# Optimization experiments

Measured on AMD Instinct MI355X. Metric: run time of the kernel, lower is better.

The kernel has to match this reference:

```python
import jax, jax.numpy as jnp
import numpy as np

N_NODES = 50000
N_EDGES = 800000
IN_DIM = 64
HID = 64
NUM_GRAPHS = 512


def _gcn_conv(x, W, b, row, col, norm, n):
    # PyG GCNConv: h = x @ W; out[col] += norm * h[row]; out += b
    h = x @ W  # [N, HID]
    msg = h[row] * norm[:, None]  # [E', HID]
    out = jax.ops.segment_sum(msg, col, num_segments=n)
    return out + b


def setup_inputs() -> dict:
    key = jax.random.key(0)
    ks = jax.random.split(key, 12)
    x = jax.random.normal(ks[0], (N_NODES, IN_DIM), dtype=jnp.float32)
    edge_index = jax.random.randint(ks[1], (2, N_EDGES), 0, N_NODES, dtype=jnp.int64)
    batch = jnp.sort(jax.random.randint(ks[2], (N_NODES,), 0, NUM_GRAPHS, dtype=jnp.int64))
    s = 0.05
    W1 = jax.random.normal(ks[3], (IN_DIM, HID), dtype=jnp.float32) * s
    b1 = jnp.zeros((HID,), dtype=jnp.float32)
    W2 = jax.random.normal(ks[4], (HID, HID), dtype=jnp.float32) * s
    b2 = jnp.zeros((HID,), dtype=jnp.float32)
    W3 = jax.random.normal(ks[5], (HID, HID), dtype=jnp.float32) * s
    b3 = jnp.zeros((HID,), dtype=jnp.float32)
    lin_W = jax.random.normal(ks[6], (HID, 1), dtype=jnp.float32) * s
    lin_b = jnp.zeros((1,), dtype=jnp.float32)
    return {"x": x, "W1": W1, "b1": b1, "W2": W2, "b2": b2, "W3": W3,
            "b3": b3, "lin_W": lin_W, "lin_b": lin_b,
            "edge_index": edge_index, "batch": batch}


def reference(x, W1, b1, W2, b2, W3, b3, lin_W, lin_b, edge_index, batch):
    n = x.shape[0]
    # add self-loops (GCNConv default add_self_loops=True)
    loop = jnp.arange(n, dtype=edge_index.dtype)
    row = jnp.concatenate([edge_index[0], loop])  # source
    col = jnp.concatenate([edge_index[1], loop])  # target (aggregation index)
    # symmetric degree normalization: deg over targets with unit weights
    deg = jax.ops.segment_sum(jnp.ones_like(col, dtype=x.dtype), col, num_segments=n)
    dinv = jnp.where(deg > 0, jax.lax.rsqrt(deg), 0.0)
    norm = dinv[row] * dinv[col]  # [E+N]

    h = jax.nn.relu(_gcn_conv(x, W1, b1, row, col, norm, n))
    h = jax.nn.relu(_gcn_conv(h, W2, b2, row, col, norm, n))
    h = _gcn_conv(h, W3, b3, row, col, norm, n)

    # global_mean_pool over batch ids
    sums = jax.ops.segment_sum(h, batch, num_segments=NUM_GRAPHS)
    cnt = jax.ops.segment_sum(jnp.ones((n,), dtype=h.dtype), batch, num_segments=NUM_GRAPHS)
    pooled = sums / jnp.maximum(cnt, 1.0)[:, None]
    # dropout p=0.5 is identity in eval mode
    return pooled @ lin_W + lin_b  # [NUM_GRAPHS, 1]
```

## Files before the change

kernel.cpp:

```cpp
#include <hip/hip_runtime.h>
#include <hip/hip_fp16.h>

#define NN 50000
#define NE 800000
#define HD 64
#define NG 512
#define NBK 196
#define NBL 196
#define M_CNT (NBK * NBL)
#define NBS 151
#define GEMM_BLOCKS 3125


__global__ __launch_bounds__(256) void bucket_count(const int* __restrict__ col,
                                                    const int* __restrict__ batch,
                                                    int* __restrict__ cnt,
                                                    int* __restrict__ counts,
                                                    int* __restrict__ beg,
                                                    int* __restrict__ endx,
                                                    float* __restrict__ pooled) {
    __shared__ int hist[256];
    int tid = threadIdx.x, blk = blockIdx.x;
    hist[tid] = 0;
    __syncthreads();
    int base = blk * 4096;
#pragma unroll
    for (int k = 0; k < 16; ++k) {
        int e = base + k * 256 + tid;
        if (e < NE) {
            int c = col[e];
            atomicAdd(&cnt[c], 1);
            atomicAdd(&hist[c >> 8], 1);
        }
    }
    int t = blk * 256 + tid;
    if (t < NG * HD) pooled[t] = 0.f;
    if (t < NN) {
        int g = batch[t];
        if (t == 0 || batch[t - 1] != g) beg[g] = t;
        if (t == NN - 1 || batch[t + 1] != g) endx[g] = t + 1;
    }
    __syncthreads();
    if (tid < NBK) counts[tid * NBL + blk] = hist[tid];
}

__global__ __launch_bounds__(256) void mscan(const int* __restrict__ src,
                                             int* __restrict__ dst) {
    __shared__ int ws[4];
    __shared__ int wsum[4];
    __shared__ int spref;
    int tid = threadIdx.x, lane = tid & 63, wid = tid >> 6;
    int lim = blockIdx.x * 256;
    int ps = 0;
    for (int k = tid; k < lim; k += 256) ps += src[k];
#pragma unroll
    for (int off = 32; off > 0; off >>= 1) ps += __shfl_down(ps, off, 64);
    if (lane == 0) wsum[wid] = ps;
    int i = lim + tid;
    int v = (i < M_CNT) ? src[i] : 0;
    int inc = v;
#pragma unroll
    for (int off = 1; off < 64; off <<= 1) {
        int t = __shfl_up(inc, off, 64);
        if (lane >= off) inc += t;
    }
    if (lane == 63) ws[wid] = inc;
    __syncthreads();
    if (tid == 0) spref = wsum[0] + wsum[1] + wsum[2] + wsum[3];
    __syncthreads();
    int woff = 0;
    for (int k = 0; k < wid; ++k) woff += ws[k];
    if (i < M_CNT) dst[i] = spref + woff + inc - v;
}

__global__ __launch_bounds__(256) void gemm1_scatter(const float* __restrict__ x,
                                                     const float* __restrict__ W1,
                                                     const int* __restrict__ cnt,
                                                     __half* __restrict__ h16,
                                                     const int* __restrict__ row,
                                                     const int* __restrict__ col,
                                                     const int* __restrict__ counts_ex,
                                                     unsigned* __restrict__ packed,
                                                     int* __restrict__ rowptr,
                                                     float* __restrict__ dinv) {
    if (blockIdx.x < GEMM_BLOCKS) {
        __shared__ float Is[16][64];
        int t = threadIdx.x;
        int c = t & 63, r4 = t >> 6;
        float wcol[64];
#pragma unroll
        for (int k = 0; k < 64; ++k) wcol[k] = W1[k * HD + c];
        int row0 = blockIdx.x * 16;
        float d0 = rsqrtf((float)(cnt[row0 + r4 + 0] + 1));
        float d1 = rsqrtf((float)(cnt[row0 + r4 + 4] + 1));
        float d2 = rsqrtf((float)(cnt[row0 + r4 + 8] + 1));
        float d3 = rsqrtf((float)(cnt[row0 + r4 + 12] + 1));
        for (int i = t; i < 16 * 64; i += 256)
            Is[i >> 6][i & 63] = x[(row0 + (i >> 6)) * HD + (i & 63)];
        __syncthreads();
        float a0 = 0.f, a1 = 0.f, a2 = 0.f, a3 = 0.f;
        const float4* i0p = (const float4*)&Is[r4 + 0][0];
        const float4* i1p = (const float4*)&Is[r4 + 4][0];
        const float4* i2p = (const float4*)&Is[r4 + 8][0];
        const float4* i3p = (const float4*)&Is[r4 + 12][0];
#pragma unroll
        for (int q = 0; q < 16; ++q) {
            float4 i0 = i0p[q], i1 = i1p[q], i2 = i2p[q], i3 = i3p[q];
            float w0 = wcol[4 * q + 0], w1 = wcol[4 * q + 1];
            float w2 = wcol[4 * q + 2], w3 = wcol[4 * q + 3];
            a0 += i0.x * w0; a0 += i0.y * w1; a0 += i0.z * w2; a0 += i0.w * w3;
            a1 += i1.x * w0; a1 += i1.y * w1; a1 += i1.z * w2; a1 += i1.w * w3;
            a2 += i2.x * w0; a2 += i2.y * w1; a2 += i2.z * w2; a2 += i2.w * w3;
            a3 += i3.x * w0; a3 += i3.y * w1; a3 += i3.z * w2; a3 += i3.w * w3;
        }
        h16[(row0 + r4 + 0) * HD + c] = __float2half(d0 * a0);
        h16[(row0 + r4 + 4) * HD + c] = __float2half(d1 * a1);
        h16[(row0 + r4 + 8) * HD + c] = __float2half(d2 * a2);
        h16[(row0 + r4 + 12) * HD + c] = __float2half(d3 * a3);
    } else if (blockIdx.x < GEMM_BLOCKS + NBL) {
        __shared__ int cur[256];
        int tid = threadIdx.x, blk = blockIdx.x - GEMM_BLOCKS;
        cur[tid] = 0;
        __syncthreads();
        int base = blk * 4096;
#pragma unroll
        for (int k = 0; k < 16; ++k) {
            int e = base + k * 256 + tid;
            if (e < NE) {
                int c = col[e], r = row[e];
                int b = c >> 8;
                int lpos = atomicAdd(&cur[b], 1);
                int pos = counts_ex[b * NBL + blk] + lpos;
                packed[pos] = (unsigned)r | ((unsigned)(c & 255) << 16);
            }
        }
    } else {
        __shared__ int ws[4];
        int b = blockIdx.x - (GEMM_BLOCKS + NBL);
        int tid = threadIdx.x, lane = tid & 63, wid = tid >> 6;
        int node = b * 256 + tid;
        int v = (node < NN) ? cnt[node] : 0;
        int inc = v;
#pragma unroll
        for (int off = 1; off < 64; off <<= 1) {
            int t = __shfl_up(inc, off, 64);
            if (lane >= off) inc += t;
        }
        if (lane == 63) ws[wid] = inc;
        __syncthreads();
        int woff = 0;
        for (int k = 0; k < wid; ++k) woff += ws[k];
        int s0 = counts_ex[b * NBL];
        if (node <= NN) rowptr[node] = s0 + woff + inc - v;
        if (node < NN) dinv[node] = rsqrtf((float)(v + 1));
    }
}

__global__ __launch_bounds__(256) void csr_fill(const unsigned* __restrict__ packed,
                                                const int* __restrict__ counts_ex,
                                                const int* __restrict__ rowptr,
                                                int* __restrict__ esrc) {
    __shared__ int lrp[256];
    __shared__ int cur[256];
    int bkt = blockIdx.x, tid = threadIdx.x;
    int s = counts_ex[bkt * NBL];
    int e = (bkt == NBK - 1) ? NE : counts_ex[(bkt + 1) * NBL];
    int node = bkt * 256 + tid;
    lrp[tid] = (node < NN) ? rowptr[node] : 0;
    cur[tid] = 0;
    __syncthreads();
    for (int j = s + tid; j < e; j += 256) {
        unsigned p = packed[j];
        int lc = (p >> 16) & 255;
        int slot = lrp[lc] + atomicAdd(&cur[lc], 1);
        esrc[slot] = (int)(p & 0xFFFF);
    }
}

template <bool POOL>
__global__ __launch_bounds__(256) void gather_fx(const __half* __restrict__ hp,
                                                 const int* __restrict__ rowptr,
                                                 const int* __restrict__ esrc,
                                                 const float* __restrict__ dinv,
                                                 const float* __restrict__ b,
                                                 const float* __restrict__ Wnext,
                                                 __half* __restrict__ hnext,
                                                 const int* __restrict__ batch,
                                                 float* __restrict__ pooled) {
    __shared__ float rowbuf[4][64];
    int tid = threadIdx.x, lane = tid & 63, wid = tid >> 6;
    int p = lane >> 5, c = lane & 31;
    int node = __builtin_amdgcn_readfirstlane(blockIdx.x * 4 + wid);
    const __half2* hv = (const __half2*)hp;

    float di = dinv[node];
    float2 self = __half22float2(hv[node * 32 + c]);
    float2 bb = ((const float2*)b)[c];

    float wcol[POOL ? 1 : 64];
    if (!POOL) {
#pragma unroll
        for (int k = 0; k < 64; ++k) wcol[k] = Wnext[k * HD + lane];
    }

    int s = rowptr[node], e = rowptr[node + 1];
    float2 acc = {0.f, 0.f};
    int j = s;
    for (; j + 8 <= e; j += 8) {
        int t0 = esrc[j + 0], t1 = esrc[j + 1], t2 = esrc[j + 2], t3 = esrc[j + 3];
        int t4 = esrc[j + 4], t5 = esrc[j + 5], t6 = esrc[j + 6], t7 = esrc[j + 7];
        int a0 = p ? t1 : t0;
        int a1 = p ? t3 : t2;
        int a2 = p ? t5 : t4;
        int a3 = p ? t7 : t6;
        float2 f0 = __half22float2(hv[a0 * 32 + c]);
        float2 f1 = __half22float2(hv[a1 * 32 + c]);
        float2 f2 = __half22float2(hv[a2 * 32 + c]);
        float2 f3 = __half22float2(hv[a3 * 32 + c]);
        acc.x += (f0.x + f1.x) + (f2.x + f3.x);
        acc.y += (f0.y + f1.y) + (f2.y + f3.y);
    }
    if (j < e) {
        int t0 = esrc[j + 0] & 0xFFFF, t1 = esrc[j + 1] & 0xFFFF;
        int t2 = esrc[j + 2] & 0xFFFF, t3 = esrc[j + 3] & 0xFFFF;
        int t4 = esrc[j + 4] & 0xFFFF, t5 = esrc[j + 5] & 0xFFFF;
        int t6 = esrc[j + 6] & 0xFFFF, t7 = esrc[j + 7] & 0xFFFF;
        int i0 = j + p, i1 = j + 2 + p, i2 = j + 4 + p, i3 = j + 6 + p;
        int a0 = p ? t1 : t0;
        int a1 = p ? t3 : t2;
        int a2 = p ? t5 : t4;
        int a3 = p ? t7 : t6;
        a0 = (i0 < e) ? a0 : t0;
        a1 = (i1 < e) ? a1 : t0;
        a2 = (i2 < e) ? a2 : t0;
        a3 = (i3 < e) ? a3 : t0;
        float m0 = (i0 < e) ? 1.f : 0.f;
        float m1 = (i1 < e) ? 1.f : 0.f;
        float m2 = (i2 < e) ? 1.f : 0.f;
        float m3 = (i3 < e) ? 1.f : 0.f;
        float2 f0 = __half22float2(hv[a0 * 32 + c]);
        float2 f1 = __half22float2(hv[a1 * 32 + c]);
        float2 f2 = __half22float2(hv[a2 * 32 + c]);
        float2 f3 = __half22float2(hv[a3 * 32 + c]);
        acc.x += m0 * f0.x + m1 * f1.x + m2 * f2.x + m3 * f3.x;
        acc.y += m0 * f0.y + m1 * f1.y + m2 * f2.y + m3 * f3.y;
    }
    acc.x += __shfl_xor(acc.x, 32, 64);
    acc.y += __shfl_xor(acc.y, 32, 64);

    if (POOL) {
        if (p == 0) {
            float vx = di * (acc.x + self.x) + bb.x;
            float vy = di * (acc.y + self.y) + bb.y;
            int g = batch[node];
            atomicAdd(&pooled[g * HD + 2 * c], vx);
            atomicAdd(&pooled[g * HD + 2 * c + 1], vy);
        }
    } else {
        if (p == 0) {
            rowbuf[wid][2 * c]     = fmaxf(di * (acc.x + self.x) + bb.x, 0.f);
            rowbuf[wid][2 * c + 1] = fmaxf(di * (acc.y + self.y) + bb.y, 0.f);
        }
        float outc = 0.f;
        const float4* rb4 = (const float4*)&rowbuf[wid][0];
#pragma unroll
        for (int jj = 0; jj < 16; ++jj) {
            float4 r = rb4[jj];
            outc += r.x * wcol[4 * jj + 0] + r.y * wcol[4 * jj + 1]
                  + r.z * wcol[4 * jj + 2] + r.w * wcol[4 * jj + 3];
        }
        hnext[(size_t)node * HD + lane] = __float2half(di * outc);
    }
}

__global__ __launch_bounds__(64) void final_kernel(const float* __restrict__ pooled,
                                                   const int* __restrict__ beg,
                                                   const int* __restrict__ endx,
                                                   const float* __restrict__ lin_W,
                                                   const float* __restrict__ lin_b,
                                                   float* __restrict__ out) {
    int g = blockIdx.x, d = threadIdx.x;
    float cnt = (float)(endx[g] - beg[g]);
    float v = pooled[g * HD + d] / fmaxf(cnt, 1.f) * lin_W[d];
#pragma unroll
    for (int off = 32; off > 0; off >>= 1) v += __shfl_down(v, off, 64);
    if (d == 0) out[g] = v + lin_b[0];
}

extern "C" void kernel_launch(void* const* d_in, const int* in_sizes, int n_in,
                              void* d_out, int out_size, void* d_ws, size_t ws_size,
                              hipStream_t stream) {
    const float* x     = (const float*)d_in[0];
    const float* W1    = (const float*)d_in[1];
    const float* b1    = (const float*)d_in[2];
    const float* W2    = (const float*)d_in[3];
    const float* b2    = (const float*)d_in[4];
    const float* W3    = (const float*)d_in[5];
    const float* b3    = (const float*)d_in[6];
    const float* lin_W = (const float*)d_in[7];
    const float* lin_b = (const float*)d_in[8];
    const int* edge_index = (const int*)d_in[9];
    const int* batch      = (const int*)d_in[10];
    const int* row = edge_index;
    const int* col = edge_index + NE;
    float* out = (float*)d_out;

    __half*   h16a      = (__half*)d_ws;
    __half*   h16b      = h16a + (size_t)NN * HD;
    int*      esrc      = (int*)(h16b + (size_t)NN * HD);
    unsigned* packed    = (unsigned*)(esrc + NE + 64);
    int*      counts    = (int*)(packed + NE);
    int*      counts_ex = counts + M_CNT;
    int*      cnt       = counts_ex + M_CNT;
    int*      rowptr    = cnt + NN;
    float*    dinv      = (float*)(rowptr + NN + 2);
    float*    pooled    = (float*)(dinv + NN);
    int*      beg       = (int*)(pooled + NG * HD);
    int*      endx      = beg + NG;

    hipMemsetAsync(cnt, 0, (size_t)NN * sizeof(int), stream);
    bucket_count<<<NBL, 256, 0, stream>>>(col, batch, cnt, counts, beg, endx,
                                          pooled);
    mscan<<<NBS, 256, 0, stream>>>(counts, counts_ex);
    gemm1_scatter<<<GEMM_BLOCKS + NBL + NBK, 256, 0, stream>>>(
        x, W1, cnt, h16a, row, col, counts_ex, packed, rowptr, dinv);
    csr_fill<<<NBK, 256, 0, stream>>>(packed, counts_ex, rowptr, esrc);

    const int GB = NN / 4;

    gather_fx<false><<<GB, 256, 0, stream>>>(h16a, rowptr, esrc, dinv, b1, W2,
                                             h16b, batch, pooled);
    gather_fx<false><<<GB, 256, 0, stream>>>(h16b, rowptr, esrc, dinv, b2, W3,
                                             h16a, batch, pooled);
    gather_fx<true><<<GB, 256, 0, stream>>>(h16a, rowptr, esrc, dinv, b3, nullptr,
                                            nullptr, batch, pooled);

    final_kernel<<<NG, 64, 0, stream>>>(pooled, beg, endx, lin_W, lin_b, out);
}
```

Measured before the change: 285.9 us.

## Fuse CSR build and first GEMM into one cooperative kernel with grid syncs

Replaces the memset plus four preprocessing launches (bucket count, scan, gemm/scatter, csr fill) with a single cooperative kernel of 256 blocks separated by grid.sync barriers. It also removes the global per-node atomic degree counts: degrees now come from a per-bucket shared histogram inside the CSR fill stage. The aim is to cut launch gaps and global atomics. The cost is that the GEMM is spread over only 256 persistent blocks and grid-wide barriers are added.

Result: slower. 427.6 us (+49.6%).

```diff
diff --git a/kernel.cpp b/kernel.cpp
--- a/kernel.cpp
+++ b/kernel.cpp
@@ -1,38 +1,51 @@
 #include <hip/hip_runtime.h>
 #include <hip/hip_fp16.h>
+#include <hip/hip_cooperative_groups.h>
+
+namespace cg = cooperative_groups;
 
 #define NN 50000
 #define NE 800000
 #define HD 64
 #define NG 512
 #define NBK 196
-#define NBL 196
-#define M_CNT (NBK * NBL)
-#define NBS 151
+#define PB  256
+#define EPB (NE / PB)
+#define M2  (PB * PB)
 #define GEMM_BLOCKS 3125
 
 
-__global__ __launch_bounds__(256) void bucket_count(const int* __restrict__ col,
-                                                    const int* __restrict__ batch,
-                                                    int* __restrict__ cnt,
-                                                    int* __restrict__ counts,
-                                                    int* __restrict__ beg,
-                                                    int* __restrict__ endx,
-                                                    float* __restrict__ pooled) {
-    __shared__ int hist[256];
+__global__ __launch_bounds__(256) void prep(const int* __restrict__ row,
+                                            const int* __restrict__ col,
+                                            const int* __restrict__ batch,
+                                            const float* __restrict__ x,
+                                            const float* __restrict__ W1,
+                                            int* __restrict__ counts,
+                                            int* __restrict__ counts_ex,
+                                            unsigned* __restrict__ packed,
+                                            int* __restrict__ rowptr,
+                                            float* __restrict__ dinv,
+                                            int* __restrict__ esrc,
+                                            __half* __restrict__ h16,
+                                            float* __restrict__ pooled,
+                                            int* __restrict__ beg,
+                                            int* __restrict__ endx) {
+    cg::grid_group grid = cg::this_grid();
+    __shared__ int   hist[256];
+    __shared__ int   lrp[256];
+    __shared__ int   ws[4];
+    __shared__ int   wsum[4];
+    __shared__ int   spref;
+    __shared__ float Is[16][64];
+
     int tid = threadIdx.x, blk = blockIdx.x;
+    int lane = tid & 63, wid = tid >> 6;
+    int lo = blk * EPB, hi = lo + EPB;
+
     hist[tid] = 0;
     __syncthreads();
-    int base = blk * 4096;
-#pragma unroll
-    for (int k = 0; k < 16; ++k) {
-        int e = base + k * 256 + tid;
-        if (e < NE) {
-            int c = col[e];
-            atomicAdd(&cnt[c], 1);
-            atomicAdd(&hist[c >> 8], 1);
-        }
-    }
+    for (int e = lo + tid; e < hi; e += 256)
+        atomicAdd(&hist[col[e] >> 8], 1);
     int t = blk * 256 + tid;
     if (t < NG * HD) pooled[t] = 0.f;
     if (t < NN) {
@@ -41,139 +54,118 @@
         if (t == NN - 1 || batch[t + 1] != g) endx[g] = t + 1;
     }
     __syncthreads();
-    if (tid < NBK) counts[tid * NBL + blk] = hist[tid];
-}
-
-__global__ __launch_bounds__(256) void mscan(const int* __restrict__ src,
-                                             int* __restrict__ dst) {
-    __shared__ int ws[4];
-    __shared__ int wsum[4];
-    __shared__ int spref;
-    int tid = threadIdx.x, lane = tid & 63, wid = tid >> 6;
-    int lim = blockIdx.x * 256;
-    int ps = 0;
-    for (int k = tid; k < lim; k += 256) ps += src[k];
-#pragma unroll
-    for (int off = 32; off > 0; off >>= 1) ps += __shfl_down(ps, off, 64);
-    if (lane == 0) wsum[wid] = ps;
-    int i = lim + tid;
-    int v = (i < M_CNT) ? src[i] : 0;
-    int inc = v;
-#pragma unroll
-    for (int off = 1; off < 64; off <<= 1) {
-        int t = __shfl_up(inc, off, 64);
-        if (lane >= off) inc += t;
-    }
-    if (lane == 63) ws[wid] = inc;
-    __syncthreads();
-    if (tid == 0) spref = wsum[0] + wsum[1] + wsum[2] + wsum[3];
-    __syncthreads();
-    int woff = 0;
-    for (int k = 0; k < wid; ++k) woff += ws[k];
-    if (i < M_CNT) dst[i] = spref + woff + inc - v;
-}
-
-__global__ __launch_bounds__(256) void gemm1_scatter(const float* __restrict__ x,
-                                                     const float* __restrict__ W1,
-                                                     const int* __restrict__ cnt,
-                                                     __half* __restrict__ h16,
-                                                     const int* __restrict__ row,
-                                                     const int* __restrict__ col,
-                                                     const int* __restrict__ counts_ex,
-                                                     unsigned* __restrict__ packed,
-                                                     int* __restrict__ rowptr,
-                                                     float* __restrict__ dinv) {
-    if (blockIdx.x < GEMM_BLOCKS) {
-        __shared__ float Is[16][64];
-        int t = threadIdx.x;
-        int c = t & 63, r4 = t >> 6;
-        float wcol[64];
-#pragma unroll
-        for (int k = 0; k < 64; ++k) wcol[k] = W1[k * HD + c];
-        int row0 = blockIdx.x * 16;
-        float d0 = rsqrtf((float)(cnt[row0 + r4 + 0] + 1));
-        float d1 = rsqrtf((float)(cnt[row0 + r4 + 4] + 1));
-        float d2 = rsqrtf((float)(cnt[row0 + r4 + 8] + 1));
-        float d3 = rsqrtf((float)(cnt[row0 + r4 + 12] + 1));
-        for (int i = t; i < 16 * 64; i += 256)
-            Is[i >> 6][i & 63] = x[(row0 + (i >> 6)) * HD + (i & 63)];
-        __syncthreads();
-        float a0 = 0.f, a1 = 0.f, a2 = 0.f, a3 = 0.f;
-        const float4* i0p = (const float4*)&Is[r4 + 0][0];
-        const float4* i1p = (const float4*)&Is[r4 + 4][0];
-        const float4* i2p = (const float4*)&Is[r4 + 8][0];
-        const float4* i3p = (const float4*)&Is[r4 + 12][0];
-#pragma unroll
-        for (int q = 0; q < 16; ++q) {
-            float4 i0 = i0p[q], i1 = i1p[q], i2 = i2p[q], i3 = i3p[q];
-            float w0 = wcol[4 * q + 0], w1 = wcol[4 * q + 1];
-            float w2 = wcol[4 * q + 2], w3 = wcol[4 * q + 3];
-            a0 += i0.x * w0; a0 += i0.y * w1; a0 += i0.z * w2; a0 += i0.w * w3;
-            a1 += i1.x * w0; a1 += i1.y * w1; a1 += i1.z * w2; a1 += i1.w * w3;
-            a2 += i2.x * w0; a2 += i2.y * w1; a2 += i2.z * w2; a2 += i2.w * w3;
-            a3 += i3.x * w0; a3 += i3.y * w1; a3 += i3.z * w2; a3 += i3.w * w3;
-        }
-        h16[(row0 + r4 + 0) * HD + c] = __float2half(d0 * a0);
-        h16[(row0 + r4 + 4) * HD + c] = __float2half(d1 * a1);
-        h16[(row0 + r4 + 8) * HD + c] = __float2half(d2 * a2);
-        h16[(row0 + r4 + 12) * HD + c] = __float2half(d3 * a3);
-    } else if (blockIdx.x < GEMM_BLOCKS + NBL) {
-        __shared__ int cur[256];
-        int tid = threadIdx.x, blk = blockIdx.x - GEMM_BLOCKS;
-        cur[tid] = 0;
-        __syncthreads();
-        int base = blk * 4096;
-#pragma unroll
-        for (int k = 0; k < 16; ++k) {
-            int e = base + k * 256 + tid;
-            if (e < NE) {
-                int c = col[e], r = row[e];
-                int b = c >> 8;
-                int lpos = atomicAdd(&cur[b], 1);
-                int pos = counts_ex[b * NBL + blk] + lpos;
-                packed[pos] = (unsigned)r | ((unsigned)(c & 255) << 16);
-            }
-        }
-    } else {
-        __shared__ int ws[4];
-        int b = blockIdx.x - (GEMM_BLOCKS + NBL);
-        int tid = threadIdx.x, lane = tid & 63, wid = tid >> 6;
-        int node = b * 256 + tid;
-        int v = (node < NN) ? cnt[node] : 0;
+    counts[tid * PB + blk] = hist[tid];
+    grid.sync();
+
+    {
+        int lim = blk * 256;
+        int ps = 0;
+        for (int k = tid; k < lim; k += 256) ps += counts[k];
+#pragma unroll
+        for (int off = 32; off > 0; off >>= 1) ps += __shfl_down(ps, off, 64);
+        if (lane == 0) wsum[wid] = ps;
+        int i = lim + tid;
+        int v = counts[i];
         int inc = v;
 #pragma unroll
         for (int off = 1; off < 64; off <<= 1) {
-            int t = __shfl_up(inc, off, 64);
-            if (lane >= off) inc += t;
+            int tt = __shfl_up(inc, off, 64);
+            if (lane >= off) inc += tt;
         }
         if (lane == 63) ws[wid] = inc;
+        __syncthreads();
+        if (tid == 0) spref = wsum[0] + wsum[1] + wsum[2] + wsum[3];
         __syncthreads();
         int woff = 0;
         for (int k = 0; k < wid; ++k) woff += ws[k];
-        int s0 = counts_ex[b * NBL];
-        if (node <= NN) rowptr[node] = s0 + woff + inc - v;
-        if (node < NN) dinv[node] = rsqrtf((float)(v + 1));
-    }
-}
-
-__global__ __launch_bounds__(256) void csr_fill(const unsigned* __restrict__ packed,
-                                                const int* __restrict__ counts_ex,
-                                                const int* __restrict__ rowptr,
-                                                int* __restrict__ esrc) {
-    __shared__ int lrp[256];
-    __shared__ int cur[256];
-    int bkt = blockIdx.x, tid = threadIdx.x;
-    int s = counts_ex[bkt * NBL];
-    int e = (bkt == NBK - 1) ? NE : counts_ex[(bkt + 1) * NBL];
-    int node = bkt * 256 + tid;
-    lrp[tid] = (node < NN) ? rowptr[node] : 0;
-    cur[tid] = 0;
+        counts_ex[i] = spref + woff + inc - v;
+    }
+    grid.sync();
+
     __syncthreads();
-    for (int j = s + tid; j < e; j += 256) {
-        unsigned p = packed[j];
-        int lc = (p >> 16) & 255;
-        int slot = lrp[lc] + atomicAdd(&cur[lc], 1);
-        esrc[slot] = (int)(p & 0xFFFF);
+    hist[tid] = 0;
+    __syncthreads();
+    for (int e = lo + tid; e < hi; e += 256) {
+        int c = col[e], r = row[e];
+        int b = c >> 8;
+        int lpos = atomicAdd(&hist[b], 1);
+        int pos = counts_ex[b * PB + blk] + lpos;
+        packed[pos] = (unsigned)r | ((unsigned)(c & 255) << 16);
+    }
+    grid.sync();
+
+    if (blk < NBK) {
+        int s = counts_ex[blk * PB];
+        int e = (blk == NBK - 1) ? NE : counts_ex[(blk + 1) * PB];
+        hist[tid] = 0;
+        __syncthreads();
+        for (int j = s + tid; j < e; j += 256)
+            atomicAdd(&hist[(packed[j] >> 16) & 255], 1);
+        __syncthreads();
+        int v = hist[tid], inc = v;
+#pragma unroll
+        for (int off = 1; off < 64; off <<= 1) {
+            int tt = __shfl_up(inc, off, 64);
+            if (lane >= off) inc += tt;
+        }
+        if (lane == 63) ws[wid] = inc;
+        __syncthreads();
+        int woff = 0;
+        for (int k = 0; k < wid; ++k) woff += ws[k];
+        int excl = s + woff + inc - v;
+        int node = blk * 256 + tid;
+        if (node < NN) {
+            rowptr[node] = excl;
+            dinv[node] = rsqrtf((float)(v + 1));
+        }
+        if (blk == 0 && tid == 0) rowptr[NN] = NE;
+        lrp[tid] = excl;
+        hist[tid] = 0;
+        __syncthreads();
+        for (int j = s + tid; j < e; j += 256) {
+            unsigned p = packed[j];
+            int lc = (p >> 16) & 255;
+            int slot = lrp[lc] + atomicAdd(&hist[lc], 1);
+            esrc[slot] = (int)(p & 0xFFFF);
+        }
+    }
+    grid.sync();
+
+    {
+        int c = tid & 63, r4 = tid >> 6;
+        float wcol[64];
+#pragma unroll
+        for (int k = 0; k < 64; ++k) wcol[k] = W1[k * HD + c];
+        for (int tile = blk; tile < GEMM_BLOCKS; tile += PB) {
+            int row0 = tile * 16;
+            float d0 = dinv[row0 + r4 + 0];
+            float d1 = dinv[row0 + r4 + 4];
+            float d2 = dinv[row0 + r4 + 8];
+            float d3 = dinv[row0 + r4 + 12];
+            for (int i = tid; i < 16 * 64; i += 256)
+                Is[i >> 6][i & 63] = x[(row0 + (i >> 6)) * HD + (i & 63)];
+            __syncthreads();
+            float a0 = 0.f, a1 = 0.f, a2 = 0.f, a3 = 0.f;
+            const float4* i0p = (const float4*)&Is[r4 + 0][0];
+            const float4* i1p = (const float4*)&Is[r4 + 4][0];
+            const float4* i2p = (const float4*)&Is[r4 + 8][0];
+            const float4* i3p = (const float4*)&Is[r4 + 12][0];
+#pragma unroll
+            for (int q = 0; q < 16; ++q) {
+                float4 i0 = i0p[q], i1 = i1p[q], i2 = i2p[q], i3 = i3p[q];
+                float w0 = wcol[4 * q + 0], w1 = wcol[4 * q + 1];
+                float w2 = wcol[4 * q + 2], w3 = wcol[4 * q + 3];
+                a0 += i0.x * w0; a0 += i0.y * w1; a0 += i0.z * w2; a0 += i0.w * w3;
+                a1 += i1.x * w0; a1 += i1.y * w1; a1 += i1.z * w2; a1 += i1.w * w3;
+                a2 += i2.x * w0; a2 += i2.y * w1; a2 += i2.z * w2; a2 += i2.w * w3;
+                a3 += i3.x * w0; a3 += i3.y * w1; a3 += i3.z * w2; a3 += i3.w * w3;
+            }
+            h16[(row0 + r4 + 0) * HD + c] = __float2half(d0 * a0);
+            h16[(row0 + r4 + 4) * HD + c] = __float2half(d1 * a1);
+            h16[(row0 + r4 + 8) * HD + c] = __float2half(d2 * a2);
+            h16[(row0 + r4 + 12) * HD + c] = __float2half(d3 * a3);
+            __syncthreads();
+        }
     }
 }
 
@@ -310,21 +302,22 @@
     int*      esrc      = (int*)(h16b + (size_t)NN * HD);
     unsigned* packed    = (unsigned*)(esrc + NE + 64);
     int*      counts    = (int*)(packed + NE);
-    int*      counts_ex = counts + M_CNT;
-    int*      cnt       = counts_ex + M_CNT;
-    int*      rowptr    = cnt + NN;
+    int*      counts_ex = counts + M2;
+    int*      rowptr    = counts_ex + M2;
     float*    dinv      = (float*)(rowptr + NN + 2);
     float*    pooled    = (float*)(dinv + NN);
     int*      beg       = (int*)(pooled + NG * HD);
     int*      endx      = beg + NG;
 
-    hipMemsetAsync(cnt, 0, (size_t)NN * sizeof(int), stream);
-    bucket_count<<<NBL, 256, 0, stream>>>(col, batch, cnt, counts, beg, endx,
-                                          pooled);
-    mscan<<<NBS, 256, 0, stream>>>(counts, counts_ex);
-    gemm1_scatter<<<GEMM_BLOCKS + NBL + NBK, 256, 0, stream>>>(
-        x, W1, cnt, h16a, row, col, counts_ex, packed, rowptr, dinv);
-    csr_fill<<<NBK, 256, 0, stream>>>(packed, counts_ex, rowptr, esrc);
+    {
+        void* args[] = {(void*)&row, (void*)&col, (void*)&batch, (void*)&x,
+                        (void*)&W1, (void*)&counts, (void*)&counts_ex,
+                        (void*)&packed, (void*)&rowptr, (void*)&dinv,
+                        (void*)&esrc, (void*)&h16a, (void*)&pooled,
+                        (void*)&beg, (void*)&endx};
+        hipLaunchCooperativeKernel((const void*)prep, dim3(PB), dim3(256),
+                                   args, 0, stream);
+    }
 
     const int GB = NN / 4;
 
```
